# Optimization experiments

Hardware: AMD Instinct MI355X
Metric: run time of the kernel (lower is better)

Reference implementation:

```python
import jax, jax.numpy as jnp
import numpy as np

ALPHA = 0.25
GAMMA = 2.0
EPS = 1e-8
COST_CLASS = 1.0
COST_BBOX = 1.0
COST_GIOU = 1.0


def segment_cw_to_t1t2(x):
    # x: [..., 2] = (center, width) -> (t1, t2)
    c, w = x[..., 0], x[..., 1]
    return jnp.stack([c - 0.5 * w, c + 0.5 * w], axis=-1)


def segment_iou(a, b):
    # a: [N, 2], b: [M, 2] -> pairwise IoU [N, M]
    lt = jnp.maximum(a[:, None, 0], b[None, :, 0])
    rb = jnp.minimum(a[:, None, 1], b[None, :, 1])
    inter = jnp.clip(rb - lt, 0.0)
    union = (a[:, 1] - a[:, 0])[:, None] + (b[:, 1] - b[:, 0])[None, :] - inter
    return inter / jnp.maximum(union, EPS)


def setup_inputs() -> dict:
    key = jax.random.key(0)
    k1, k2, k3, k4, k5, k6 = jax.random.split(key, 6)
    bs, Q, n_cls, M = 16, 2000, 80, 1024
    pred_logits = jax.random.normal(k1, (bs, Q, n_cls), dtype=jnp.float32)
    # boxes layout: [t1, t2, center, width] with t1<=t2 and width>0 (valid segments)
    p_t = jnp.sort(jax.random.uniform(k2, (bs, Q, 2), dtype=jnp.float32), axis=-1)
    p_cw = jax.random.uniform(k3, (bs, Q, 2), dtype=jnp.float32) * jnp.array([1.0, 0.5]) + jnp.array([0.0, 0.05])
    pred_boxes = jnp.concatenate([p_t, p_cw], axis=-1)
    t_t = jnp.sort(jax.random.uniform(k4, (M, 2), dtype=jnp.float32), axis=-1)
    t_cw = jax.random.uniform(k5, (M, 2), dtype=jnp.float32) * jnp.array([1.0, 0.5]) + jnp.array([0.0, 0.05])
    tgt_bbox = jnp.concatenate([t_t, t_cw], axis=-1)
    tgt_ids = jax.random.randint(k6, (M,), 0, n_cls, dtype=jnp.int64 if jax.config.jax_enable_x64 else jnp.int32)
    return {"pred_logits": pred_logits, "pred_boxes": pred_boxes,
            "tgt_ids": tgt_ids, "tgt_bbox": tgt_bbox}


def reference(pred_logits, pred_boxes, tgt_ids, tgt_bbox):
    bs, Q, _ = pred_logits.shape
    out_prob = jax.nn.softmax(pred_logits.reshape(bs * Q, -1), axis=-1)  # [bs*Q, n_cls]
    out_bbox = pred_boxes.reshape(bs * Q, 4)
    # focal-style classification cost
    neg_cost = (1.0 - ALPHA) * out_prob ** GAMMA * (-jnp.log1p(-out_prob + EPS))
    pos_cost = ALPHA * (1.0 - out_prob) ** GAMMA * (-jnp.log(out_prob + EPS))
    cost_class = pos_cost[:, tgt_ids] - neg_cost[:, tgt_ids]  # [bs*Q, M]
    # L1 box cost (cdist p=1)
    cost_bbox = jnp.sum(jnp.abs(out_bbox[:, None, :] - tgt_bbox[None, :, :]), axis=-1)
    # GIoU-style cost: average of IoU over (c,w)->t1t2 segments and raw t1t2 segments
    cost_giou = -(segment_iou(segment_cw_to_t1t2(out_bbox[:, 2:]), segment_cw_to_t1t2(tgt_bbox[:, 2:]))
                  + segment_iou(out_bbox[:, :2], tgt_bbox[:, :2])) / 2.0
    C = COST_BBOX * cost_bbox + COST_CLASS * cost_class + COST_GIOU * cost_giou
    return C.reshape(bs, Q, -1)
```

## Files before the change

### kernel.cpp

```cpp
#include <hip/hip_runtime.h>
#include <math.h>

#define ALPHA 0.25f
#define EPS 1e-8f

constexpr int NCLS = 80;
constexpr int Mn = 1024;
constexpr int RPB = 8;

__global__ __launch_bounds__(256) void matcher_kernel(
    const float* __restrict__ logits,
    const float* __restrict__ pboxes,
    const int*   __restrict__ tids,
    const float* __restrict__ tboxes,
    float* __restrict__ out)
{
    __shared__ float cls[RPB][NCLS];
    __shared__ float rowd[RPB][8];

    const int tid  = threadIdx.x;
    const int row0 = blockIdx.x * RPB;

    const int j0 = tid * 4;
    float4 tb[4]; int id[4]; float tt1[4], tt2[4], twr[4];
    #pragma unroll
    for (int k = 0; k < 4; ++k) {
        tb[k] = *(const float4*)(tboxes + (size_t)(j0 + k) * 4);
        id[k] = tids[j0 + k];
    }

    if (tid < 160) {
        ((float4*)&cls[0][0])[tid] =
            ((const float4*)(logits + (size_t)row0 * NCLS))[tid];
    }
    if (tid < RPB) {
        float4 pb = *(const float4*)(pboxes + (size_t)(row0 + tid) * 4);
        rowd[tid][0] = pb.x;
        rowd[tid][1] = pb.y;
        rowd[tid][2] = pb.z;
        rowd[tid][3] = pb.w;
        rowd[tid][4] = pb.z - 0.5f * pb.w;
        rowd[tid][5] = pb.z + 0.5f * pb.w;
        rowd[tid][6] = pb.y - pb.x;
        rowd[tid][7] = 0.0f;
    }
    #pragma unroll
    for (int k = 0; k < 4; ++k) {
        tt1[k] = tb[k].z - 0.5f * tb[k].w;
        tt2[k] = tb[k].z + 0.5f * tb[k].w;
        twr[k] = tb[k].y - tb[k].x;
    }
    __syncthreads();

    {
        const int r = tid >> 5;
        const int c = tid & 31;
        const int c2 = (c < 16) ? c + 64 : c;
        float l0 = cls[r][c];
        float l1 = cls[r][c + 32];
        float l2 = cls[r][c2];
        float e0 = __expf(l0);
        float e1 = __expf(l1);
        float e2 = (c < 16) ? __expf(l2) : 0.0f;
        float s = e0 + e1 + e2;
        #pragma unroll
        for (int off = 16; off; off >>= 1) s += __shfl_xor(s, off);
        float inv_s = __builtin_amdgcn_rcpf(s);
        float p0 = e0 * inv_s, p1 = e1 * inv_s, p2 = e2 * inv_s;

        float o0 = 1.0f - p0, o1 = 1.0f - p1, o2 = 1.0f - p2;
        float cc0 = ALPHA * o0 * o0 * (-__logf(p0 + EPS))
                  - (1.0f - ALPHA) * p0 * p0 * (-__logf(o0 + EPS));
        float cc1 = ALPHA * o1 * o1 * (-__logf(p1 + EPS))
                  - (1.0f - ALPHA) * p1 * p1 * (-__logf(o1 + EPS));
        float cc2 = ALPHA * o2 * o2 * (-__logf(p2 + EPS))
                  - (1.0f - ALPHA) * p2 * p2 * (-__logf(o2 + EPS));
        cls[r][c]      = cc0;
        cls[r][c + 32] = cc1;
        if (c < 16) cls[r][c + 64] = cc2;
    }
    __syncthreads();

    #pragma unroll
    for (int r = 0; r < RPB; ++r) {
        float4 ra = *(float4*)&rowd[r][0];
        float4 rb = *(float4*)&rowd[r][4];
        float4 res;
        #pragma unroll
        for (int k = 0; k < 4; ++k) {
            float db = fabsf(ra.x - tb[k].x) + fabsf(ra.y - tb[k].y)
                     + fabsf(ra.z - tb[k].z) + fabsf(ra.w - tb[k].w);
            float lt    = fmaxf(rb.x, tt1[k]);
            float rr    = fminf(rb.y, tt2[k]);
            float inter = fmaxf(rr - lt, 0.0f);
            float uni   = ra.w + tb[k].w - inter;
            float iou1  = inter * __builtin_amdgcn_rcpf(fmaxf(uni, EPS));
            float lt2    = fmaxf(ra.x, tb[k].x);
            float rr2    = fminf(ra.y, tb[k].y);
            float inter2 = fmaxf(rr2 - lt2, 0.0f);
            float uni2   = rb.z + twr[k] - inter2;
            float iou2   = inter2 * __builtin_amdgcn_rcpf(fmaxf(uni2, EPS));

            (&res.x)[k] = db + cls[r][id[k]] - 0.5f * (iou1 + iou2);
        }
        *(float4*)(out + (size_t)(row0 + r) * Mn + j0) = res;
    }
}

extern "C" void kernel_launch(void* const* d_in, const int* in_sizes, int n_in,
                              void* d_out, int out_size, void* d_ws, size_t ws_size,
                              hipStream_t stream) {
    const float* logits = (const float*)d_in[0];
    const float* pboxes = (const float*)d_in[1];
    const int*   tids   = (const int*)d_in[2];
    const float* tboxes = (const float*)d_in[3];
    float* out = (float*)d_out;

    const int total_rows = in_sizes[0] / NCLS;
    const int nblocks = total_rows / RPB;
    matcher_kernel<<<nblocks, 256, 0, stream>>>(logits, pboxes, tids, tboxes, out);
}
```

Baseline: 39.33 us.

## Reformulate IoU algebra, merge reciprocals, use nontemporal stores and occupancy hint

Rewrites the segment-intersection math as sums and differences of absolute values so the L1 terms are shared with the IoU terms. The two reciprocals are merged into one division over a common denominator. Pred boxes are now read from global memory inside the row loop instead of being staged in shared memory, and the loop is partially unrolled. Adds nontemporal output stores and a minimum-blocks launch bound. Merging the divisions and using the abs-based forms changes rounding slightly, and a product of denominators near EPS could lose precision.

Measured after the change: 35.84 us. -8.9%, faster.

```diff
diff --git a/kernel.cpp b/kernel.cpp
--- a/kernel.cpp
+++ b/kernel.cpp
@@ -4,11 +4,13 @@
 #define ALPHA 0.25f
 #define EPS 1e-8f
 
+typedef float f4v __attribute__((ext_vector_type(4)));
+
 constexpr int NCLS = 80;
 constexpr int Mn = 1024;
 constexpr int RPB = 8;
 
-__global__ __launch_bounds__(256) void matcher_kernel(
+__global__ __launch_bounds__(256, 5) void matcher_kernel(
     const float* __restrict__ logits,
     const float* __restrict__ pboxes,
     const int*   __restrict__ tids,
@@ -16,39 +18,27 @@
     float* __restrict__ out)
 {
     __shared__ float cls[RPB][NCLS];
-    __shared__ float rowd[RPB][8];
 
     const int tid  = threadIdx.x;
     const int row0 = blockIdx.x * RPB;
 
     const int j0 = tid * 4;
-    float4 tb[4]; int id[4]; float tt1[4], tt2[4], twr[4];
+    float t1[4], t2[4], tc[4], th[4], wr[4];
+    int id[4];
     #pragma unroll
     for (int k = 0; k < 4; ++k) {
-        tb[k] = *(const float4*)(tboxes + (size_t)(j0 + k) * 4);
+        float4 b = *(const float4*)(tboxes + (size_t)(j0 + k) * 4);
+        t1[k] = b.x;
+        t2[k] = b.y;
+        tc[k] = b.z;
+        th[k] = 0.5f * b.w;
+        wr[k] = b.y - b.x;
         id[k] = tids[j0 + k];
     }
 
     if (tid < 160) {
         ((float4*)&cls[0][0])[tid] =
             ((const float4*)(logits + (size_t)row0 * NCLS))[tid];
-    }
-    if (tid < RPB) {
-        float4 pb = *(const float4*)(pboxes + (size_t)(row0 + tid) * 4);
-        rowd[tid][0] = pb.x;
-        rowd[tid][1] = pb.y;
-        rowd[tid][2] = pb.z;
-        rowd[tid][3] = pb.w;
-        rowd[tid][4] = pb.z - 0.5f * pb.w;
-        rowd[tid][5] = pb.z + 0.5f * pb.w;
-        rowd[tid][6] = pb.y - pb.x;
-        rowd[tid][7] = 0.0f;
-    }
-    #pragma unroll
-    for (int k = 0; k < 4; ++k) {
-        tt1[k] = tb[k].z - 0.5f * tb[k].w;
-        tt2[k] = tb[k].z + 0.5f * tb[k].w;
-        twr[k] = tb[k].y - tb[k].x;
     }
     __syncthreads();
 
@@ -67,7 +57,6 @@
         for (int off = 16; off; off >>= 1) s += __shfl_xor(s, off);
         float inv_s = __builtin_amdgcn_rcpf(s);
         float p0 = e0 * inv_s, p1 = e1 * inv_s, p2 = e2 * inv_s;
-
         float o0 = 1.0f - p0, o1 = 1.0f - p1, o2 = 1.0f - p2;
         float cc0 = ALPHA * o0 * o0 * (-__logf(p0 + EPS))
                   - (1.0f - ALPHA) * p0 * p0 * (-__logf(o0 + EPS));
@@ -81,29 +70,33 @@
     }
     __syncthreads();
 
-    #pragma unroll
+    #pragma unroll 2
     for (int r = 0; r < RPB; ++r) {
-        float4 ra = *(float4*)&rowd[r][0];
-        float4 rb = *(float4*)&rowd[r][4];
-        float4 res;
+        const float4 pb = *(const float4*)(pboxes + (size_t)(row0 + r) * 4);
+        const float pwr = pb.y - pb.x;
+        const float phw = 0.5f * pb.w;
+
+        f4v res;
         #pragma unroll
         for (int k = 0; k < 4; ++k) {
-            float db = fabsf(ra.x - tb[k].x) + fabsf(ra.y - tb[k].y)
-                     + fabsf(ra.z - tb[k].z) + fabsf(ra.w - tb[k].w);
-            float lt    = fmaxf(rb.x, tt1[k]);
-            float rr    = fminf(rb.y, tt2[k]);
-            float inter = fmaxf(rr - lt, 0.0f);
-            float uni   = ra.w + tb[k].w - inter;
-            float iou1  = inter * __builtin_amdgcn_rcpf(fmaxf(uni, EPS));
-            float lt2    = fmaxf(ra.x, tb[k].x);
-            float rr2    = fminf(ra.y, tb[k].y);
-            float inter2 = fmaxf(rr2 - lt2, 0.0f);
-            float uni2   = rb.z + twr[k] - inter2;
-            float iou2   = inter2 * __builtin_amdgcn_rcpf(fmaxf(uni2, EPS));
-
-            (&res.x)[k] = db + cls[r][id[k]] - 0.5f * (iou1 + iou2);
+            float d1 = pb.x - t1[k];
+            float d2 = pb.y - t2[k];
+            float dc = pb.z - tc[k];
+            float dw = phw - th[k];
+            float ab = fabsf(d1) + fabsf(d2);
+            float db = ab + fmaf(fabsf(dw), 2.0f, fabsf(dc));
+            float P1 = fmaf(2.0f, th[k], pb.w);
+            float A1 = fmaxf(P1 - (fabsf(dc - dw) + fabsf(dc + dw)), 0.0f);
+            float D1 = fmaxf(fmaf(2.0f, P1, -A1), 2.0f * EPS);
+            float P2 = pwr + wr[k];
+            float A2 = fmaxf(P2 - ab, 0.0f);
+            float D2 = fmaxf(fmaf(2.0f, P2, -A2), 2.0f * EPS);
+            float num = A1 * D2 + A2 * D1;
+            float inv = __builtin_amdgcn_rcpf(D1 * D2);
+            res[k] = fmaf(num * inv, -0.5f, db + cls[r][id[k]]);
         }
-        *(float4*)(out + (size_t)(row0 + r) * Mn + j0) = res;
+        __builtin_nontemporal_store(res,
+            (f4v*)(out + (size_t)(row0 + r) * Mn + j0));
     }
 }
 
```
